# Optimization experiments

Measured on AMD Instinct MI355X. Metric: run time of the kernel, lower is better.

## Reference

```python
import jax, jax.numpy as jnp
import numpy as np

EMBED_DIM = 1024
HEADS = 16
HEAD_DIM = EMBED_DIM // HEADS


def setup_inputs() -> dict:
    key = jax.random.key(0)
    ks = jax.random.split(key, 9)
    D = EMBED_DIM
    s = 1.0 / np.sqrt(D)
    x = jax.random.normal(ks[0], (4, 2048, D), dtype=jnp.float32)
    Wq = jax.random.uniform(ks[1], (D, D), jnp.float32, -s, s)
    bq = jnp.zeros((D,), jnp.float32)
    Wk = jax.random.uniform(ks[2], (D, D), jnp.float32, -s, s)
    bk = jnp.zeros((D,), jnp.float32)
    Wv = jax.random.uniform(ks[3], (D, D), jnp.float32, -s, s)
    bv = jnp.zeros((D,), jnp.float32)
    Wo = jax.random.uniform(ks[4], (D, D), jnp.float32, -s, s)
    bo = jnp.zeros((D,), jnp.float32)
    gamma = jnp.ones((D,), jnp.float32)
    beta = jnp.zeros((D,), jnp.float32)
    return {"x": x, "Wq": Wq, "bq": bq, "Wk": Wk, "bk": bk,
            "Wv": Wv, "bv": bv, "Wo": Wo, "bo": bo,
            "gamma": gamma, "beta": beta}


def reference(x, Wq, bq, Wk, bk, Wv, bv, Wo, bo, gamma, beta):
    B, S, D = x.shape
    H, Dh = HEADS, HEAD_DIM
    # projections -> [B, H, S, Dh]
    q = (x @ Wq + bq).reshape(B, S, H, Dh).transpose(0, 2, 1, 3)
    k = (x @ Wk + bk).reshape(B, S, H, Dh).transpose(0, 2, 1, 3)
    v = (x @ Wv + bv).reshape(B, S, H, Dh).transpose(0, 2, 1, 3)
    scores = jnp.einsum('bhqd,bhkd->bhqk', q, k) / jnp.sqrt(jnp.float32(Dh))
    attn = jax.nn.softmax(scores, axis=-1)  # dropout is identity in eval
    ctx = jnp.einsum('bhqk,bhkd->bhqd', attn, v)
    ctx = ctx.transpose(0, 2, 1, 3).reshape(B, S, D)
    out = ctx @ Wo + bo
    # residual + LayerNorm (eps=1e-5, torch default)
    h = out + x
    mu = jnp.mean(h, axis=-1, keepdims=True)
    var = jnp.mean(jnp.square(h - mu), axis=-1, keepdims=True)
    return (h - mu) * jax.lax.rsqrt(var + 1e-5) * gamma + beta
```

## Files before the change

### kernel.cpp

```cpp
#include <hip/hip_runtime.h>
#include <hip/hip_bf16.h>
#include <stdint.h>

typedef short sh4 __attribute__((ext_vector_type(4)));
typedef short sh8 __attribute__((ext_vector_type(8)));
typedef float fl4 __attribute__((ext_vector_type(4)));
typedef float f32x4 __attribute__((ext_vector_type(4)));
typedef float f32x16 __attribute__((ext_vector_type(16)));
typedef uint32_t u32x4 __attribute__((ext_vector_type(4)));

static __device__ __forceinline__ short f2bf(float f) {
  union { float f; uint32_t u; } v;
  v.f = f;
  uint32_t r = v.u + 0x7fffu + ((v.u >> 16) & 1u);
  return (short)(r >> 16);
}

static __device__ __forceinline__ uint32_t cvt_pk_bf16(float a, float b) {
  uint32_t r;
  asm("v_cvt_pk_bf16_f32 %0, %1, %2" : "=v"(r) : "v"(a), "v"(b));
  return r;
}

static __device__ __forceinline__ void pl32swap(uint32_t& a, uint32_t& b) {
  asm volatile("v_permlane32_swap_b32 %0, %1" : "+v"(a), "+v"(b));
}

static __device__ __forceinline__ void gload_lds16(const void* g, void* l) {
  __builtin_amdgcn_global_load_lds((const __attribute__((address_space(1))) void*)g,
                                   (__attribute__((address_space(3))) void*)l, 16, 0, 0);
}

__global__ __launch_bounds__(256) void k_wt(const float* __restrict__ Wq, const float* __restrict__ Wk,
                                            const float* __restrict__ Wv, const float* __restrict__ Wo,
                                            short* __restrict__ Tq, short* __restrict__ Tk,
                                            short* __restrict__ Tv, short* __restrict__ To,
                                            const float* __restrict__ x, short* __restrict__ xbf) {
  if (blockIdx.z == 4) {
    int tid = threadIdx.y * 32 + threadIdx.x;
    size_t base = ((size_t)blockIdx.y * 32 + blockIdx.x) * 8192;
#pragma unroll
    for (int i = 0; i < 8; i++) {
      size_t idx = base + (size_t)i * 1024 + tid * 4;
      fl4 v = *(const fl4*)&x[idx];
      sh4 r;
#pragma unroll
      for (int j = 0; j < 4; j++) r[j] = f2bf(v[j]);
      *(sh4*)&xbf[idx] = r;
    }
    return;
  }
  const float* W = blockIdx.z == 0 ? Wq : blockIdx.z == 1 ? Wk : blockIdx.z == 2 ? Wv : Wo;
  short* T = blockIdx.z == 0 ? Tq : blockIdx.z == 1 ? Tk : blockIdx.z == 2 ? Tv : To;
  __shared__ float tile[32][33];
  int n0 = blockIdx.x * 32, k0 = blockIdx.y * 32;
  int tx = threadIdx.x, ty = threadIdx.y;
#pragma unroll
  for (int p = 0; p < 4; p++) tile[ty + 8 * p][tx] = W[(size_t)(k0 + ty + 8 * p) * 1024 + n0 + tx];
  __syncthreads();
#pragma unroll
  for (int p = 0; p < 4; p++) T[(size_t)(n0 + ty + 8 * p) * 1024 + k0 + tx] = f2bf(tile[tx][ty + 8 * p]);
}

#define PIPE_LOOP(STAGE_BODY, COMPUTE_BODY, VM)                          \
  STAGE_BODY(0, 0);                                                      \
  STAGE_BODY(1, 1);                                                      \
  {                                                                      \
    int bufc = 0, bufs = 2;                                              \
    for (int it = 0; it < 32; it++) {                                    \
      if (it < 31)                                                       \
        asm volatile("s_waitcnt vmcnt(" VM ")" ::: "memory");            \
      else                                                               \
        asm volatile("s_waitcnt vmcnt(0)" ::: "memory");                 \
      __builtin_amdgcn_s_barrier();                                      \
      if (it + 2 < 32) { STAGE_BODY(it + 2, bufs); }                     \
      __builtin_amdgcn_sched_barrier(0);                                 \
      { int buf = bufc; COMPUTE_BODY }                                   \
      bufc = bufc == 2 ? 0 : bufc + 1;                                   \
      bufs = bufs == 2 ? 0 : bufs + 1;                                   \
      asm volatile("" ::: "memory");                                     \
    }                                                                    \
  }

__global__ __launch_bounds__(512, 4) void k_qk(const short* __restrict__ A, const short* __restrict__ WT2,
                                               const float* __restrict__ bq, const float* __restrict__ bk,
                                               short* __restrict__ Qo, short* __restrict__ Ko, float qscale) {
  __shared__ __align__(16) short As[3][256 * 32];
  __shared__ __align__(16) short Bs[3][128 * 32];
  const int xcd = blockIdx.x & 7, j = blockIdx.x >> 3;
  const int m0 = (j >> 1) * 256, n0 = (xcd * 2 + (j & 1)) * 128;
  const int sec = n0 >> 10;
  const float* bias = sec == 0 ? bq : bk;
  short* Out = sec == 0 ? Qo : Ko;
  const float scale = sec == 0 ? qscale : 1.f;
  const int t = threadIdx.x;
  const int lane = t & 63, w = t >> 6;
  const int wr = w >> 1, wc = w & 1;
  const int l15 = lane & 15, g = lane >> 4;
  f32x4 acc[4][4];
#pragma unroll
  for (int mi = 0; mi < 4; mi++)
#pragma unroll
    for (int ni = 0; ni < 4; ni++) acc[mi][ni] = (f32x4){0.f, 0.f, 0.f, 0.f};

#define QK_STAGE(kt, buf)                                                                     \
  {                                                                                           \
    int r0 = w * 32;                                                                          \
    _Pragma("unroll") for (int i = 0; i < 2; i++) {                                           \
      int row = r0 + i * 16 + (lane >> 2);                                                    \
      gload_lds16(&A[(size_t)(m0 + row) * 1024 + (kt) * 32 + (lane & 3) * 8],                 \
                  &As[buf][(r0 + i * 16) * 32]);                                              \
    }                                                                                         \
    int brow = w * 16 + (lane >> 2);                                                          \
    gload_lds16(&WT2[(size_t)(n0 + brow) * 1024 + (kt) * 32 + (lane & 3) * 8],                \
                &Bs[buf][(w * 16) * 32]);                                                     \
  }

#define QK_COMPUTE                                                                            \
  sh8 a[4], b[4];                                                                             \
  _Pragma("unroll") for (int i = 0; i < 4; i++)                                               \
      a[i] = *(sh8*)&As[buf][(wr * 64 + i * 16 + l15) * 32 + g * 8];                          \
  _Pragma("unroll") for (int i = 0; i < 4; i++)                                               \
      b[i] = *(sh8*)&Bs[buf][(wc * 64 + i * 16 + l15) * 32 + g * 8];                          \
  _Pragma("unroll") for (int mi = 0; mi < 4; mi++)                                            \
      _Pragma("unroll") for (int ni = 0; ni < 4; ni++)                                        \
          acc[mi][ni] = __builtin_amdgcn_mfma_f32_16x16x32_bf16(b[ni], a[mi], acc[mi][ni], 0, 0, 0);

  PIPE_LOOP(QK_STAGE, QK_COMPUTE, "3")

#pragma unroll
  for (int ni = 0; ni < 4; ni++) {
    int nbase = n0 + wc * 64 + ni * 16 + g * 4;
    int nn0 = nbase & 1023;
    fl4 bv4 = *(const fl4*)&bias[nn0];
    int h = nn0 >> 6, dh0 = nn0 & 63;
#pragma unroll
    for (int mi = 0; mi < 4; mi++) {
      int m = m0 + wr * 64 + mi * 16 + l15;
      int bb = m >> 11, s = m & 2047;
      uint2 dd;
      dd.x = cvt_pk_bf16((acc[mi][ni][0] + bv4[0]) * scale, (acc[mi][ni][1] + bv4[1]) * scale);
      dd.y = cvt_pk_bf16((acc[mi][ni][2] + bv4[2]) * scale, (acc[mi][ni][3] + bv4[3]) * scale);
      *(uint2*)&Out[(((size_t)bb * 16 + h) * 2048 + s) * 64 + dh0] = dd;
    }
  }
}

__global__ __launch_bounds__(256) void k_v(const short* __restrict__ A, const short* __restrict__ WTv,
                                           const float* __restrict__ bv, short* __restrict__ Vo) {
  __shared__ __align__(16) short As[3][128 * 32];
  __shared__ __align__(16) short Bs[3][128 * 32];
  const int xcd = blockIdx.x & 7, j = blockIdx.x >> 3;
  const int m0 = (xcd + 8 * (j & 7)) * 128, n0 = (j >> 3) * 128;
  const int t = threadIdx.x;
  const int lane = t & 63, w = t >> 6;
  const int wr = w >> 1, wc = w & 1;
  const int l15 = lane & 15, g = lane >> 4;
  f32x4 acc[4][4];
#pragma unroll
  for (int mi = 0; mi < 4; mi++)
#pragma unroll
    for (int ni = 0; ni < 4; ni++) acc[mi][ni] = (f32x4){0.f, 0.f, 0.f, 0.f};

#define V_STAGE(kt, buf)                                                                      \
  {                                                                                           \
    int r0 = w * 32;                                                                          \
    _Pragma("unroll") for (int i = 0; i < 2; i++) {                                           \
      int row = r0 + i * 16 + (lane >> 2);                                                    \
      gload_lds16(&A[(size_t)(m0 + row) * 1024 + (kt) * 32 + (lane & 3) * 8],                 \
                  &As[buf][(r0 + i * 16) * 32]);                                              \
      gload_lds16(&WTv[(size_t)(n0 + row) * 1024 + (kt) * 32 + (lane & 3) * 8],               \
                  &Bs[buf][(r0 + i * 16) * 32]);                                              \
    }                                                                                         \
  }

#define V_COMPUTE                                                                             \
  sh8 a[4], b[4];                                                                             \
  _Pragma("unroll") for (int i = 0; i < 4; i++)                                               \
      a[i] = *(sh8*)&As[buf][(wr * 64 + i * 16 + l15) * 32 + g * 8];                          \
  _Pragma("unroll") for (int i = 0; i < 4; i++)                                               \
      b[i] = *(sh8*)&Bs[buf][(wc * 64 + i * 16 + l15) * 32 + g * 8];                          \
  _Pragma("unroll") for (int mi = 0; mi < 4; mi++)                                            \
      _Pragma("unroll") for (int ni = 0; ni < 4; ni++)                                        \
          acc[mi][ni] = __builtin_amdgcn_mfma_f32_16x16x32_bf16(a[mi], b[ni], acc[mi][ni], 0, 0, 0);

  PIPE_LOOP(V_STAGE, V_COMPUTE, "4")

#pragma unroll
  for (int ni = 0; ni < 4; ni++) {
    int col = n0 + wc * 64 + ni * 16 + l15;
    int nn = col & 1023;
    float bvv = bv[nn];
    int h = nn >> 6, dh = nn & 63;
#pragma unroll
    for (int mi = 0; mi < 4; mi++) {
      int mr = m0 + wr * 64 + mi * 16 + g * 4;
      int bb = mr >> 11, s = mr & 2047;
      uint2 dd;
      dd.x = cvt_pk_bf16(acc[mi][ni][0] + bvv, acc[mi][ni][1] + bvv);
      dd.y = cvt_pk_bf16(acc[mi][ni][2] + bvv, acc[mi][ni][3] + bvv);
      *(uint2*)&Vo[(((size_t)bb * 16 + h) * 64 + dh) * 2048 + s] = dd;
    }
  }
}

__global__ __launch_bounds__(256) void k_oproj(const short* __restrict__ A, const short* __restrict__ BT,
                                               const float* __restrict__ bias, const float* __restrict__ X,
                                               float* __restrict__ Out) {
  __shared__ __align__(16) short As[3][128 * 32];
  __shared__ __align__(16) short Bs[3][128 * 32];
  const int xcd = blockIdx.x & 7, j = blockIdx.x >> 3;
  const int m0 = (xcd + 8 * (j & 7)) * 128, n0 = (j >> 3) * 128;
  const int t = threadIdx.x;
  const int lane = t & 63, w = t >> 6;
  const int wr = w >> 1, wc = w & 1;
  const int l15 = lane & 15, g = lane >> 4;
  f32x4 acc[4][4];
#pragma unroll
  for (int mi = 0; mi < 4; mi++)
#pragma unroll
    for (int ni = 0; ni < 4; ni++) acc[mi][ni] = (f32x4){0.f, 0.f, 0.f, 0.f};

#define O_STAGE(kt, buf)                                                                      \
  {                                                                                           \
    int r0 = w * 32;                                                                          \
    _Pragma("unroll") for (int i = 0; i < 2; i++) {                                           \
      int row = r0 + i * 16 + (lane >> 2);                                                    \
      gload_lds16(&A[(size_t)(m0 + row) * 1024 + (kt) * 32 + (lane & 3) * 8],                 \
                  &As[buf][(r0 + i * 16) * 32]);                                              \
      gload_lds16(&BT[(size_t)(n0 + row) * 1024 + (kt) * 32 + (lane & 3) * 8],                \
                  &Bs[buf][(r0 + i * 16) * 32]);                                              \
    }                                                                                         \
  }

#define O_COMPUTE                                                                             \
  sh8 a[4], b[4];                                                                             \
  _Pragma("unroll") for (int i = 0; i < 4; i++)                                               \
      a[i] = *(sh8*)&As[buf][(wr * 64 + i * 16 + l15) * 32 + g * 8];                          \
  _Pragma("unroll") for (int i = 0; i < 4; i++)                                               \
      b[i] = *(sh8*)&Bs[buf][(wc * 64 + i * 16 + l15) * 32 + g * 8];                          \
  _Pragma("unroll") for (int mi = 0; mi < 4; mi++)                                            \
      _Pragma("unroll") for (int ni = 0; ni < 4; ni++)                                        \
          acc[mi][ni] = __builtin_amdgcn_mfma_f32_16x16x32_bf16(b[ni], a[mi], acc[mi][ni], 0, 0, 0);

  PIPE_LOOP(O_STAGE, O_COMPUTE, "4")

#pragma unroll
  for (int ni = 0; ni < 4; ni++) {
    int nbase = n0 + wc * 64 + ni * 16 + g * 4;
    fl4 bv4 = *(const fl4*)&bias[nbase];
#pragma unroll
    for (int mi = 0; mi < 4; mi++) {
      int m = m0 + wr * 64 + mi * 16 + l15;
      fl4 xv = *(const fl4*)&X[(size_t)m * 1024 + nbase];
      fl4 r;
#pragma unroll
      for (int e = 0; e < 4; e++) r[e] = acc[mi][ni][e] + bv4[e] + xv[e];
      *(fl4*)&Out[(size_t)m * 1024 + nbase] = r;
    }
  }
}

__global__ __launch_bounds__(512, 4) void k_attn(const short* __restrict__ Q, const short* __restrict__ K,
                                                 const short* __restrict__ Vt, short* __restrict__ CTX) {
  const int nid = (blockIdx.x & 7) * 64 + (blockIdx.x >> 3);
  const int qbi = nid & 7, h = (nid >> 3) & 15, b = nid >> 7;
  const int q0 = qbi * 256;
  const size_t ho = (((size_t)b * 16 + h) * 2048) * 64;
  const short* Qh = Q + ho;
  const short* Kh = K + ho;
  const short* Vh = Vt + ho;
  __shared__ __align__(16) short Ks[4][8 * 512];
  __shared__ __align__(16) short Vs[5][8 * 512];
  const int t = threadIdx.x, lane = t & 63, w = t >> 6;
  const int l31 = lane & 31, hi = lane >> 5;

  sh8 qreg[4];
#pragma unroll
  for (int ks = 0; ks < 4; ks++)
    qreg[ks] = *(const sh8*)&Qh[(size_t)(q0 + w * 32 + l31) * 64 + ks * 16 + hi * 8];

  f32x16 zinit;
#pragma unroll
  for (int r = 0; r < 16; r++) zinit[r] = 0.f;

  f32x16 oc0 = zinit, oc1 = zinit;
  float l_s = 0.f;
  u32x4 pwp[4];

  auto stageK = [&](int kt, int buf) {
    gload_lds16(&Kh[(size_t)(kt * 64 + (w >> 2) * 32 + l31) * 64 + (w & 3) * 16 + hi * 8],
                (char*)&Ks[buf][0] + w * 1024);
  };
  auto stageV = [&](int kt, int buf) {
    gload_lds16(&Vh[(size_t)((w >> 2) * 32 + l31) * 2048 + kt * 64 + (w & 3) * 16 + hi * 8],
                (char*)&Vs[buf][0] + w * 1024);
  };

  stageK(0, 0); stageV(0, 0);
  stageK(1, 1); stageV(1, 1);
  stageK(2, 2); stageV(2, 2);
  int vs = 3, vp = 4;

  for (int kt = 0; kt < 32; kt++) {
    if (kt < 30)
      asm volatile("s_waitcnt vmcnt(4)" ::: "memory");
    else if (kt == 30)
      asm volatile("s_waitcnt vmcnt(2)" ::: "memory");
    else
      asm volatile("s_waitcnt vmcnt(0)" ::: "memory");
    __builtin_amdgcn_s_barrier();
    if (kt + 3 < 32) { stageK(kt + 3, (kt + 3) & 3); stageV(kt + 3, vs); }
    __builtin_amdgcn_sched_barrier(0);
    const int kbuf = kt & 3;

    f32x16 s0, s1;
    __builtin_amdgcn_s_setprio(1);
#pragma unroll
    for (int ks = 0; ks < 4; ks++) {
      sh8 ak0 = *(sh8*)((char*)&Ks[kbuf][0] + ks * 1024 + lane * 16);
      sh8 ak1 = *(sh8*)((char*)&Ks[kbuf][0] + (4 + ks) * 1024 + lane * 16);
      if (ks == 0) {
        s0 = __builtin_amdgcn_mfma_f32_32x32x16_bf16(ak0, qreg[0], zinit, 0, 0, 0);
        s1 = __builtin_amdgcn_mfma_f32_32x32x16_bf16(ak1, qreg[0], zinit, 0, 0, 0);
      } else {
        s0 = __builtin_amdgcn_mfma_f32_32x32x16_bf16(ak0, qreg[ks], s0, 0, 0, 0);
        s1 = __builtin_amdgcn_mfma_f32_32x32x16_bf16(ak1, qreg[ks], s1, 0, 0, 0);
      }
    }

    if (kt > 0) {
#pragma unroll
      for (int ks = 0; ks < 4; ks++) {
        sh8 pb = __builtin_bit_cast(sh8, pwp[ks]);
        sh8 av0 = *(sh8*)((char*)&Vs[vp][0] + ks * 1024 + lane * 16);
        sh8 av1 = *(sh8*)((char*)&Vs[vp][0] + (4 + ks) * 1024 + lane * 16);
        oc0 = __builtin_amdgcn_mfma_f32_32x32x16_bf16(av0, pb, oc0, 0, 0, 0);
        oc1 = __builtin_amdgcn_mfma_f32_32x32x16_bf16(av1, pb, oc1, 0, 0, 0);
      }
    }
    __builtin_amdgcn_s_setprio(0);

#pragma unroll
    for (int r = 0; r < 16; r++) s0[r] = __builtin_amdgcn_exp2f(s0[r]);
#pragma unroll
    for (int r = 0; r < 16; r++) s1[r] = __builtin_amdgcn_exp2f(s1[r]);
    {
      float t0[8];
#pragma unroll
      for (int r = 0; r < 8; r++) t0[r] = (s0[2 * r] + s0[2 * r + 1]) + (s1[2 * r] + s1[2 * r + 1]);
      float u0 = (t0[0] + t0[1]) + (t0[2] + t0[3]);
      float u1 = (t0[4] + t0[5]) + (t0[6] + t0[7]);
      l_s += u0 + u1;
    }

    {
      uint32_t a0 = cvt_pk_bf16(s0[0], s0[1]), a1 = cvt_pk_bf16(s0[2], s0[3]);
      uint32_t b0 = cvt_pk_bf16(s0[4], s0[5]), b1 = cvt_pk_bf16(s0[6], s0[7]);
      uint32_t c0 = cvt_pk_bf16(s0[8], s0[9]), c1 = cvt_pk_bf16(s0[10], s0[11]);
      uint32_t d0 = cvt_pk_bf16(s0[12], s0[13]), d1 = cvt_pk_bf16(s0[14], s0[15]);
      pl32swap(a0, b0); pl32swap(a1, b1); pl32swap(c0, d0); pl32swap(c1, d1);
      pwp[0] = (u32x4){a0, a1, b0, b1};
      pwp[1] = (u32x4){c0, c1, d0, d1};
      a0 = cvt_pk_bf16(s1[0], s1[1]); a1 = cvt_pk_bf16(s1[2], s1[3]);
      b0 = cvt_pk_bf16(s1[4], s1[5]); b1 = cvt_pk_bf16(s1[6], s1[7]);
      c0 = cvt_pk_bf16(s1[8], s1[9]); c1 = cvt_pk_bf16(s1[10], s1[11]);
      d0 = cvt_pk_bf16(s1[12], s1[13]); d1 = cvt_pk_bf16(s1[14], s1[15]);
      pl32swap(a0, b0); pl32swap(a1, b1); pl32swap(c0, d0); pl32swap(c1, d1);
      pwp[2] = (u32x4){a0, a1, b0, b1};
      pwp[3] = (u32x4){c0, c1, d0, d1};
    }
    vp = vp == 4 ? 0 : vp + 1;
    vs = vs == 4 ? 0 : vs + 1;
    asm volatile("" ::: "memory");
  }

  {
    __builtin_amdgcn_s_setprio(1);
#pragma unroll
    for (int ks = 0; ks < 4; ks++) {
      sh8 pb = __builtin_bit_cast(sh8, pwp[ks]);
      sh8 av0 = *(sh8*)((char*)&Vs[vp][0] + ks * 1024 + lane * 16);
      sh8 av1 = *(sh8*)((char*)&Vs[vp][0] + (4 + ks) * 1024 + lane * 16);
      oc0 = __builtin_amdgcn_mfma_f32_32x32x16_bf16(av0, pb, oc0, 0, 0, 0);
      oc1 = __builtin_amdgcn_mfma_f32_32x32x16_bf16(av1, pb, oc1, 0, 0, 0);
    }
    __builtin_amdgcn_s_setprio(0);
  }

  l_s += __shfl_xor(l_s, 32);
  float li = 1.f / l_s;
  int s = q0 + w * 32 + l31;
  size_t obase = (((size_t)b * 2048 + s) * 16 + h) * 64;
#pragma unroll
  for (int rq = 0; rq < 4; rq++) {
    uint2 dd;
    dd.x = cvt_pk_bf16(oc0[4 * rq] * li, oc0[4 * rq + 1] * li);
    dd.y = cvt_pk_bf16(oc0[4 * rq + 2] * li, oc0[4 * rq + 3] * li);
    *(uint2*)&CTX[obase + rq * 8 + hi * 4] = dd;
    dd.x = cvt_pk_bf16(oc1[4 * rq] * li, oc1[4 * rq + 1] * li);
    dd.y = cvt_pk_bf16(oc1[4 * rq + 2] * li, oc1[4 * rq + 3] * li);
    *(uint2*)&CTX[obase + 32 + rq * 8 + hi * 4] = dd;
  }
}

__global__ __launch_bounds__(256) void k_ln(float* __restrict__ Out, const float* __restrict__ gamma,
                                            const float* __restrict__ beta) {
  int row = blockIdx.x * 4 + (threadIdx.x >> 6);
  int lane = threadIdx.x & 63;
  float* p = Out + (size_t)row * 1024;
  fl4 v[4];
  float s = 0.f, s2 = 0.f;
#pragma unroll
  for (int j = 0; j < 4; j++) {
    v[j] = *(fl4*)&p[lane * 4 + j * 256];
#pragma unroll
    for (int e = 0; e < 4; e++) { s += v[j][e]; s2 += v[j][e] * v[j][e]; }
  }
#pragma unroll
  for (int off = 1; off < 64; off <<= 1) {
    s += __shfl_xor(s, off);
    s2 += __shfl_xor(s2, off);
  }
  float mu = s * (1.f / 1024.f);
  float var = s2 * (1.f / 1024.f) - mu * mu;
  float inv = rsqrtf(var + 1e-5f);
#pragma unroll
  for (int j = 0; j < 4; j++) {
    fl4 r;
#pragma unroll
    for (int e = 0; e < 4; e++) {
      int c = lane * 4 + j * 256 + e;
      r[e] = (v[j][e] - mu) * inv * gamma[c] + beta[c];
    }
    *(fl4*)&p[lane * 4 + j * 256] = r;
  }
}

extern "C" void kernel_launch(void* const* d_in, const int* in_sizes, int n_in,
                              void* d_out, int out_size, void* d_ws, size_t ws_size,
                              hipStream_t stream) {
  (void)in_sizes; (void)n_in; (void)out_size; (void)ws_size;
  const float* x = (const float*)d_in[0];
  const float* Wq = (const float*)d_in[1];
  const float* bq = (const float*)d_in[2];
  const float* Wk = (const float*)d_in[3];
  const float* bk = (const float*)d_in[4];
  const float* Wv = (const float*)d_in[5];
  const float* bv = (const float*)d_in[6];
  const float* Wo = (const float*)d_in[7];
  const float* bo = (const float*)d_in[8];
  const float* gamma = (const float*)d_in[9];
  const float* beta = (const float*)d_in[10];
  float* out = (float*)d_out;
  char* ws = (char*)d_ws;
  short* xbf = (short*)(ws);
  short* wtq = (short*)(ws + (16ull << 20));
  short* wtk = (short*)(ws + (18ull << 20));
  short* wtv = (short*)(ws + (20ull << 20));
  short* wto = (short*)(ws + (22ull << 20));
  short* qb  = (short*)(ws + (24ull << 20));
  short* kbuf = (short*)(ws + (40ull << 20));
  short* vbuf = (short*)(ws + (56ull << 20));
  short* ctx = (short*)(ws + (72ull << 20));

  const float QSCALE = 0.125f * 1.44269504088896f;

  k_wt<<<dim3(32, 32, 5), dim3(32, 8), 0, stream>>>(Wq, Wk, Wv, Wo, wtq, wtk, wtv, wto, x, xbf);
  k_qk<<<512, 512, 0, stream>>>(xbf, wtq, bq, bk, qb, kbuf, QSCALE);
  k_v<<<512, 256, 0, stream>>>(xbf, wtv, bv, vbuf);
  k_attn<<<512, 512, 0, stream>>>(qb, kbuf, vbuf, ctx);
  k_oproj<<<512, 256, 0, stream>>>(ctx, wto, bo, x, out);
  k_ln<<<2048, 256, 0, stream>>>(out, gamma, beta);
}
```

Baseline: 205.0 us.

## Process two query tiles per wave in attention to reuse K/V LDS reads

The attention kernel now runs 4 waves per block instead of 8, and each wave handles 64 query rows (two 32-row tiles) instead of 32. Each K/V fragment read from LDS therefore feeds twice as many MFMAs, and each wave stages two K/V chunks per tile. The prefetch depth drops from 3 tiles ahead to 2, with K and V ring buffers cut to 3 and 4 slots. In exchange, register pressure doubles for accumulators and P fragments, there are fewer waves per block, and the shallower pipeline can expose more global-load latency.

Result: no change. 206.3 us (+0.6%).

```diff
diff --git a/kernel.cpp b/kernel.cpp
--- a/kernel.cpp
+++ b/kernel.cpp
@@ -261,7 +261,7 @@
   }
 }
 
-__global__ __launch_bounds__(512, 4) void k_attn(const short* __restrict__ Q, const short* __restrict__ K,
+__global__ __launch_bounds__(256, 2) void k_attn(const short* __restrict__ Q, const short* __restrict__ K,
                                                  const short* __restrict__ Vt, short* __restrict__ CTX) {
   const int nid = (blockIdx.x & 7) * 64 + (blockIdx.x >> 3);
   const int qbi = nid & 7, h = (nid >> 3) & 15, b = nid >> 7;
@@ -270,73 +270,81 @@
   const short* Qh = Q + ho;
   const short* Kh = K + ho;
   const short* Vh = Vt + ho;
-  __shared__ __align__(16) short Ks[4][8 * 512];
-  __shared__ __align__(16) short Vs[5][8 * 512];
+  __shared__ __align__(16) short Ks[3][8 * 512];
+  __shared__ __align__(16) short Vs[4][8 * 512];
   const int t = threadIdx.x, lane = t & 63, w = t >> 6;
   const int l31 = lane & 31, hi = lane >> 5;
 
-  sh8 qreg[4];
-#pragma unroll
-  for (int ks = 0; ks < 4; ks++)
-    qreg[ks] = *(const sh8*)&Qh[(size_t)(q0 + w * 32 + l31) * 64 + ks * 16 + hi * 8];
+  sh8 qA[4], qB[4];
+#pragma unroll
+  for (int ks = 0; ks < 4; ks++) {
+    qA[ks] = *(const sh8*)&Qh[(size_t)(q0 + w * 64 + l31) * 64 + ks * 16 + hi * 8];
+    qB[ks] = *(const sh8*)&Qh[(size_t)(q0 + w * 64 + 32 + l31) * 64 + ks * 16 + hi * 8];
+  }
 
   f32x16 zinit;
 #pragma unroll
   for (int r = 0; r < 16; r++) zinit[r] = 0.f;
 
-  f32x16 oc0 = zinit, oc1 = zinit;
-  float l_s = 0.f;
-  u32x4 pwp[4];
-
-  auto stageK = [&](int kt, int buf) {
-    gload_lds16(&Kh[(size_t)(kt * 64 + (w >> 2) * 32 + l31) * 64 + (w & 3) * 16 + hi * 8],
-                (char*)&Ks[buf][0] + w * 1024);
+  f32x16 oc00 = zinit, oc01 = zinit, oc10 = zinit, oc11 = zinit;
+  float lA = 0.f, lB = 0.f;
+  u32x4 pwpA[4], pwpB[4];
+
+  auto stage = [&](int kt, int kb, int vb) {
+#pragma unroll
+    for (int i = 0; i < 2; i++) {
+      int c = 2 * w + i;
+      gload_lds16(&Kh[(size_t)(kt * 64 + (c >> 2) * 32 + l31) * 64 + (c & 3) * 16 + hi * 8],
+                  (char*)&Ks[kb][0] + c * 1024);
+      gload_lds16(&Vh[(size_t)((c >> 2) * 32 + l31) * 2048 + kt * 64 + (c & 3) * 16 + hi * 8],
+                  (char*)&Vs[vb][0] + c * 1024);
+    }
   };
-  auto stageV = [&](int kt, int buf) {
-    gload_lds16(&Vh[(size_t)((w >> 2) * 32 + l31) * 2048 + kt * 64 + (w & 3) * 16 + hi * 8],
-                (char*)&Vs[buf][0] + w * 1024);
-  };
-
-  stageK(0, 0); stageV(0, 0);
-  stageK(1, 1); stageV(1, 1);
-  stageK(2, 2); stageV(2, 2);
-  int vs = 3, vp = 4;
+
+  stage(0, 0, 0);
+  stage(1, 1, 1);
+  int kbufc = 0, kbufs = 2;
+  int vp = 3;
 
   for (int kt = 0; kt < 32; kt++) {
-    if (kt < 30)
+    if (kt < 31)
       asm volatile("s_waitcnt vmcnt(4)" ::: "memory");
-    else if (kt == 30)
-      asm volatile("s_waitcnt vmcnt(2)" ::: "memory");
     else
       asm volatile("s_waitcnt vmcnt(0)" ::: "memory");
     __builtin_amdgcn_s_barrier();
-    if (kt + 3 < 32) { stageK(kt + 3, (kt + 3) & 3); stageV(kt + 3, vs); }
+    if (kt + 2 < 32) stage(kt + 2, kbufs, (kt + 2) & 3);
     __builtin_amdgcn_sched_barrier(0);
-    const int kbuf = kt & 3;
-
-    f32x16 s0, s1;
+
+    f32x16 s0, s1, s2, s3;
     __builtin_amdgcn_s_setprio(1);
 #pragma unroll
     for (int ks = 0; ks < 4; ks++) {
-      sh8 ak0 = *(sh8*)((char*)&Ks[kbuf][0] + ks * 1024 + lane * 16);
-      sh8 ak1 = *(sh8*)((char*)&Ks[kbuf][0] + (4 + ks) * 1024 + lane * 16);
+      sh8 ak0 = *(sh8*)((char*)&Ks[kbufc][0] + ks * 1024 + lane * 16);
+      sh8 ak1 = *(sh8*)((char*)&Ks[kbufc][0] + (4 + ks) * 1024 + lane * 16);
       if (ks == 0) {
-        s0 = __builtin_amdgcn_mfma_f32_32x32x16_bf16(ak0, qreg[0], zinit, 0, 0, 0);
-        s1 = __builtin_amdgcn_mfma_f32_32x32x16_bf16(ak1, qreg[0], zinit, 0, 0, 0);
+        s0 = __builtin_amdgcn_mfma_f32_32x32x16_bf16(ak0, qA[0], zinit, 0, 0, 0);
+        s1 = __builtin_amdgcn_mfma_f32_32x32x16_bf16(ak1, qA[0], zinit, 0, 0, 0);
+        s2 = __builtin_amdgcn_mfma_f32_32x32x16_bf16(ak0, qB[0], zinit, 0, 0, 0);
+        s3 = __builtin_amdgcn_mfma_f32_32x32x16_bf16(ak1, qB[0], zinit, 0, 0, 0);
       } else {
-        s0 = __builtin_amdgcn_mfma_f32_32x32x16_bf16(ak0, qreg[ks], s0, 0, 0, 0);
-        s1 = __builtin_amdgcn_mfma_f32_32x32x16_bf16(ak1, qreg[ks], s1, 0, 0, 0);
+        s0 = __builtin_amdgcn_mfma_f32_32x32x16_bf16(ak0, qA[ks], s0, 0, 0, 0);
+        s1 = __builtin_amdgcn_mfma_f32_32x32x16_bf16(ak1, qA[ks], s1, 0, 0, 0);
+        s2 = __builtin_amdgcn_mfma_f32_32x32x16_bf16(ak0, qB[ks], s2, 0, 0, 0);
+        s3 = __builtin_amdgcn_mfma_f32_32x32x16_bf16(ak1, qB[ks], s3, 0, 0, 0);
       }
     }
 
     if (kt > 0) {
 #pragma unroll
       for (int ks = 0; ks < 4; ks++) {
-        sh8 pb = __builtin_bit_cast(sh8, pwp[ks]);
+        sh8 pa = __builtin_bit_cast(sh8, pwpA[ks]);
+        sh8 pbq = __builtin_bit_cast(sh8, pwpB[ks]);
         sh8 av0 = *(sh8*)((char*)&Vs[vp][0] + ks * 1024 + lane * 16);
         sh8 av1 = *(sh8*)((char*)&Vs[vp][0] + (4 + ks) * 1024 + lane * 16);
-        oc0 = __builtin_amdgcn_mfma_f32_32x32x16_bf16(av0, pb, oc0, 0, 0, 0);
-        oc1 = __builtin_amdgcn_mfma_f32_32x32x16_bf16(av1, pb, oc1, 0, 0, 0);
+        oc00 = __builtin_amdgcn_mfma_f32_32x32x16_bf16(av0, pa, oc00, 0, 0, 0);
+        oc01 = __builtin_amdgcn_mfma_f32_32x32x16_bf16(av1, pa, oc01, 0, 0, 0);
+        oc10 = __builtin_amdgcn_mfma_f32_32x32x16_bf16(av0, pbq, oc10, 0, 0, 0);
+        oc11 = __builtin_amdgcn_mfma_f32_32x32x16_bf16(av1, pbq, oc11, 0, 0, 0);
       }
     }
     __builtin_amdgcn_s_setprio(0);
@@ -349,29 +357,49 @@
       float t0[8];
 #pragma unroll
       for (int r = 0; r < 8; r++) t0[r] = (s0[2 * r] + s0[2 * r + 1]) + (s1[2 * r] + s1[2 * r + 1]);
-      float u0 = (t0[0] + t0[1]) + (t0[2] + t0[3]);
-      float u1 = (t0[4] + t0[5]) + (t0[6] + t0[7]);
-      l_s += u0 + u1;
-    }
-
-    {
+      lA += ((t0[0] + t0[1]) + (t0[2] + t0[3])) + ((t0[4] + t0[5]) + (t0[6] + t0[7]));
       uint32_t a0 = cvt_pk_bf16(s0[0], s0[1]), a1 = cvt_pk_bf16(s0[2], s0[3]);
       uint32_t b0 = cvt_pk_bf16(s0[4], s0[5]), b1 = cvt_pk_bf16(s0[6], s0[7]);
       uint32_t c0 = cvt_pk_bf16(s0[8], s0[9]), c1 = cvt_pk_bf16(s0[10], s0[11]);
       uint32_t d0 = cvt_pk_bf16(s0[12], s0[13]), d1 = cvt_pk_bf16(s0[14], s0[15]);
       pl32swap(a0, b0); pl32swap(a1, b1); pl32swap(c0, d0); pl32swap(c1, d1);
-      pwp[0] = (u32x4){a0, a1, b0, b1};
-      pwp[1] = (u32x4){c0, c1, d0, d1};
+      pwpA[0] = (u32x4){a0, a1, b0, b1};
+      pwpA[1] = (u32x4){c0, c1, d0, d1};
       a0 = cvt_pk_bf16(s1[0], s1[1]); a1 = cvt_pk_bf16(s1[2], s1[3]);
       b0 = cvt_pk_bf16(s1[4], s1[5]); b1 = cvt_pk_bf16(s1[6], s1[7]);
       c0 = cvt_pk_bf16(s1[8], s1[9]); c1 = cvt_pk_bf16(s1[10], s1[11]);
       d0 = cvt_pk_bf16(s1[12], s1[13]); d1 = cvt_pk_bf16(s1[14], s1[15]);
       pl32swap(a0, b0); pl32swap(a1, b1); pl32swap(c0, d0); pl32swap(c1, d1);
-      pwp[2] = (u32x4){a0, a1, b0, b1};
-      pwp[3] = (u32x4){c0, c1, d0, d1};
-    }
-    vp = vp == 4 ? 0 : vp + 1;
-    vs = vs == 4 ? 0 : vs + 1;
+      pwpA[2] = (u32x4){a0, a1, b0, b1};
+      pwpA[3] = (u32x4){c0, c1, d0, d1};
+    }
+#pragma unroll
+    for (int r = 0; r < 16; r++) s2[r] = __builtin_amdgcn_exp2f(s2[r]);
+#pragma unroll
+    for (int r = 0; r < 16; r++) s3[r] = __builtin_amdgcn_exp2f(s3[r]);
+    {
+      float t0[8];
+#pragma unroll
+      for (int r = 0; r < 8; r++) t0[r] = (s2[2 * r] + s2[2 * r + 1]) + (s3[2 * r] + s3[2 * r + 1]);
+      lB += ((t0[0] + t0[1]) + (t0[2] + t0[3])) + ((t0[4] + t0[5]) + (t0[6] + t0[7]));
+      uint32_t a0 = cvt_pk_bf16(s2[0], s2[1]), a1 = cvt_pk_bf16(s2[2], s2[3]);
+      uint32_t b0 = cvt_pk_bf16(s2[4], s2[5]), b1 = cvt_pk_bf16(s2[6], s2[7]);
+      uint32_t c0 = cvt_pk_bf16(s2[8], s2[9]), c1 = cvt_pk_bf16(s2[10], s2[11]);
+      uint32_t d0 = cvt_pk_bf16(s2[12], s2[13]), d1 = cvt_pk_bf16(s2[14], s2[15]);
+      pl32swap(a0, b0); pl32swap(a1, b1); pl32swap(c0, d0); pl32swap(c1, d1);
+      pwpB[0] = (u32x4){a0, a1, b0, b1};
+      pwpB[1] = (u32x4){c0, c1, d0, d1};
+      a0 = cvt_pk_bf16(s3[0], s3[1]); a1 = cvt_pk_bf16(s3[2], s3[3]);
+      b0 = cvt_pk_bf16(s3[4], s3[5]); b1 = cvt_pk_bf16(s3[6], s3[7]);
+      c0 = cvt_pk_bf16(s3[8], s3[9]); c1 = cvt_pk_bf16(s3[10], s3[11]);
+      d0 = cvt_pk_bf16(s3[12], s3[13]); d1 = cvt_pk_bf16(s3[14], s3[15]);
+      pl32swap(a0, b0); pl32swap(a1, b1); pl32swap(c0, d0); pl32swap(c1, d1);
+      pwpB[2] = (u32x4){a0, a1, b0, b1};
+      pwpB[3] = (u32x4){c0, c1, d0, d1};
+    }
+    kbufc = kbufc == 2 ? 0 : kbufc + 1;
+    kbufs = kbufs == 2 ? 0 : kbufs + 1;
+    vp = (vp + 1) & 3;
     asm volatile("" ::: "memory");
   }
 
@@ -379,28 +407,48 @@
     __builtin_amdgcn_s_setprio(1);
 #pragma unroll
     for (int ks = 0; ks < 4; ks++) {
-      sh8 pb = __builtin_bit_cast(sh8, pwp[ks]);
+      sh8 pa = __builtin_bit_cast(sh8, pwpA[ks]);
+      sh8 pbq = __builtin_bit_cast(sh8, pwpB[ks]);
       sh8 av0 = *(sh8*)((char*)&Vs[vp][0] + ks * 1024 + lane * 16);
       sh8 av1 = *(sh8*)((char*)&Vs[vp][0] + (4 + ks) * 1024 + lane * 16);
-      oc0 = __builtin_amdgcn_mfma_f32_32x32x16_bf16(av0, pb, oc0, 0, 0, 0);
-      oc1 = __builtin_amdgcn_mfma_f32_32x32x16_bf16(av1, pb, oc1, 0, 0, 0);
+      oc00 = __builtin_amdgcn_mfma_f32_32x32x16_bf16(av0, pa, oc00, 0, 0, 0);
+      oc01 = __builtin_amdgcn_mfma_f32_32x32x16_bf16(av1, pa, oc01, 0, 0, 0);
+      oc10 = __builtin_amdgcn_mfma_f32_32x32x16_bf16(av0, pbq, oc10, 0, 0, 0);
+      oc11 = __builtin_amdgcn_mfma_f32_32x32x16_bf16(av1, pbq, oc11, 0, 0, 0);
     }
     __builtin_amdgcn_s_setprio(0);
   }
 
-  l_s += __shfl_xor(l_s, 32);
-  float li = 1.f / l_s;
-  int s = q0 + w * 32 + l31;
-  size_t obase = (((size_t)b * 2048 + s) * 16 + h) * 64;
-#pragma unroll
-  for (int rq = 0; rq < 4; rq++) {
-    uint2 dd;
-    dd.x = cvt_pk_bf16(oc0[4 * rq] * li, oc0[4 * rq + 1] * li);
-    dd.y = cvt_pk_bf16(oc0[4 * rq + 2] * li, oc0[4 * rq + 3] * li);
-    *(uint2*)&CTX[obase + rq * 8 + hi * 4] = dd;
-    dd.x = cvt_pk_bf16(oc1[4 * rq] * li, oc1[4 * rq + 1] * li);
-    dd.y = cvt_pk_bf16(oc1[4 * rq + 2] * li, oc1[4 * rq + 3] * li);
-    *(uint2*)&CTX[obase + 32 + rq * 8 + hi * 4] = dd;
+  lA += __shfl_xor(lA, 32);
+  lB += __shfl_xor(lB, 32);
+  float liA = 1.f / lA, liB = 1.f / lB;
+  {
+    int s = q0 + w * 64 + l31;
+    size_t obase = (((size_t)b * 2048 + s) * 16 + h) * 64;
+#pragma unroll
+    for (int rq = 0; rq < 4; rq++) {
+      uint2 dd;
+      dd.x = cvt_pk_bf16(oc00[4 * rq] * liA, oc00[4 * rq + 1] * liA);
+      dd.y = cvt_pk_bf16(oc00[4 * rq + 2] * liA, oc00[4 * rq + 3] * liA);
+      *(uint2*)&CTX[obase + rq * 8 + hi * 4] = dd;
+      dd.x = cvt_pk_bf16(oc01[4 * rq] * liA, oc01[4 * rq + 1] * liA);
+      dd.y = cvt_pk_bf16(oc01[4 * rq + 2] * liA, oc01[4 * rq + 3] * liA);
+      *(uint2*)&CTX[obase + 32 + rq * 8 + hi * 4] = dd;
+    }
+  }
+  {
+    int s = q0 + w * 64 + 32 + l31;
+    size_t obase = (((size_t)b * 2048 + s) * 16 + h) * 64;
+#pragma unroll
+    for (int rq = 0; rq < 4; rq++) {
+      uint2 dd;
+      dd.x = cvt_pk_bf16(oc10[4 * rq] * liB, oc10[4 * rq + 1] * liB);
+      dd.y = cvt_pk_bf16(oc10[4 * rq + 2] * liB, oc10[4 * rq + 3] * liB);
+      *(uint2*)&CTX[obase + rq * 8 + hi * 4] = dd;
+      dd.x = cvt_pk_bf16(oc11[4 * rq] * liB, oc11[4 * rq + 1] * liB);
+      dd.y = cvt_pk_bf16(oc11[4 * rq + 2] * liB, oc11[4 * rq + 3] * liB);
+      *(uint2*)&CTX[obase + 32 + rq * 8 + hi * 4] = dd;
+    }
   }
 }
 
@@ -469,7 +517,7 @@
   k_wt<<<dim3(32, 32, 5), dim3(32, 8), 0, stream>>>(Wq, Wk, Wv, Wo, wtq, wtk, wtv, wto, x, xbf);
   k_qk<<<512, 512, 0, stream>>>(xbf, wtq, bq, bk, qb, kbuf, QSCALE);
   k_v<<<512, 256, 0, stream>>>(xbf, wtv, bv, vbuf);
-  k_attn<<<512, 512, 0, stream>>>(qb, kbuf, vbuf, ctx);
+  k_attn<<<512, 256, 0, stream>>>(qb, kbuf, vbuf, ctx);
   k_oproj<<<512, 256, 0, stream>>>(ctx, wto, bo, x, out);
   k_ln<<<2048, 256, 0, stream>>>(out, gamma, beta);
 }
```
